# Performance work log

Hardware: AMD Instinct MI355X
Metric: run time of the kernel (lower is better)

The kernel has to match this reference:

```python
import jax, jax.numpy as jnp
import numpy as np

B, C, H, W, NW = 4, 32, 64, 64, 64
VMAX = 1.0


def _sunflower_mu_stddev(n, vmax, alpha=1.0):
    # sunflower seed arrangement on the complex plane (matches torch source)
    b = np.round(alpha * np.sqrt(n))
    phi = (np.sqrt(5.0) + 1.0) * 0.5
    k = np.arange(1, n + 1, dtype=np.float64)
    r = np.where(k > n - b, 1.0, np.sqrt(k - 0.5) / np.sqrt(n - (b + 1.0) / 2.0))
    theta = 2.0 * np.pi * k / phi ** 2
    mu = (r * np.cos(theta) + 1j * r * np.sin(theta)) * vmax
    # nearest-neighbor distance (replaces sklearn NearestNeighbors exactly)
    X = np.stack((mu.real, mu.imag), -1)  # (n,2)
    D = np.linalg.norm(X[:, None, :] - X[None, :, :], axis=-1)
    np.fill_diagonal(D, np.inf)
    nn_d = D.min(axis=1)
    stddev = (nn_d * nn_d).astype(np.float32)
    return mu.real.astype(np.float32), mu.imag.astype(np.float32), stddev


def setup_inputs() -> dict:
    key = jax.random.key(0)
    k1, k2, k3, k4 = jax.random.split(key, 4)
    mu_r, mu_i, stddev = _sunflower_mu_stddev(NW, VMAX)
    return {
        "x_real": jax.random.normal(k1, (B, C, H, W), dtype=jnp.float32),
        "x_imag": jax.random.normal(k2, (B, C, H, W), dtype=jnp.float32),
        "w_real": jax.random.normal(k3, (C, NW), dtype=jnp.float32) * 0.1,
        "w_imag": jax.random.normal(k4, (C, NW), dtype=jnp.float32) * 0.1,
        "b_real": jnp.zeros((1, C, 1), dtype=jnp.float32),
        "b_imag": jnp.zeros((1, C, 1), dtype=jnp.float32),
        "mu_real": jnp.asarray(mu_r),
        "mu_imag": jnp.asarray(mu_i),
        "stddev": jnp.asarray(stddev),
    }


def reference(x_real, x_imag, w_real, w_imag, b_real, b_imag, mu_real, mu_imag, stddev):
    Bb, Cc, Hh, Ww = x_real.shape
    # (B,C,HW,1) complex input vs (1,1,1,NW) complex centers
    xr = x_real.reshape(Bb, Cc, -1, 1)
    xi = x_imag.reshape(Bb, Cc, -1, 1)
    dr = xr - mu_real.reshape(1, 1, 1, -1)
    di = xi - mu_imag.reshape(1, 1, 1, -1)
    # conj(dist)*dist = |dist|^2 (real); exp of it is real-valued
    rbf = jnp.exp(-(dr * dr + di * di) / (2.0 * stddev))  # (B,C,HW,NW) real
    # complex channel-weighted reduction + complex bias
    out_r = jnp.einsum('abcd,bd->abc', rbf, w_real) + b_real
    out_i = jnp.einsum('abcd,bd->abc', rbf, w_imag) + b_imag
    # return real/imag stacked on last axis: (B,C,H,W,2)
    out = jnp.stack([out_r.reshape(Bb, Cc, Hh, Ww), out_i.reshape(Bb, Cc, Hh, Ww)], axis=-1)
    return out
```

## Files before the change

kernel.cpp:

```cpp
#include <hip/hip_runtime.h>

#define NB 4
#define NC 32
#define HW 4096
#define NW 64

#define PPT 4
#define TPB 256
#define PPB (PPT * TPB)
#define TILES (HW / PPB)

__global__ __launch_bounds__(TPB) void rbf_kernel(
    const float* __restrict__ x_real, const float* __restrict__ x_imag,
    const float* __restrict__ w_real, const float* __restrict__ w_imag,
    const float* __restrict__ b_real, const float* __restrict__ b_imag,
    const float* __restrict__ mu_real, const float* __restrict__ mu_imag,
    const float* __restrict__ stddev, float* __restrict__ out)
{
    const int bc   = blockIdx.x / TILES;
    const int tile = blockIdx.x % TILES;
    const int c    = bc % NC;
    const int t    = threadIdx.x;

    __shared__ float s_mu_r[NW], s_mu_i[NW], s_coef[NW], s_wr[NW], s_wi[NW];
    if (t < NW) {
        s_mu_r[t] = mu_real[t];
        s_mu_i[t] = mu_imag[t];
        s_coef[t] = -1.4426950408889634f / (2.0f * stddev[t]);
        s_wr[t]   = w_real[c * NW + t];
        s_wi[t]   = w_imag[c * NW + t];
    }
    __syncthreads();

    const int base = bc * HW + tile * PPB + t;

    float xr[PPT], xi[PPT], ar[PPT], ai[PPT];
#pragma unroll
    for (int p = 0; p < PPT; ++p) {
        xr[p] = x_real[base + p * TPB];
        xi[p] = x_imag[base + p * TPB];
        ar[p] = 0.0f;
        ai[p] = 0.0f;
    }

#pragma unroll 8
    for (int k = 0; k < NW; ++k) {
        const float mr = s_mu_r[k];
        const float mi = s_mu_i[k];
        const float cf = s_coef[k];
        const float wr = s_wr[k];
        const float wi = s_wi[k];
#pragma unroll
        for (int p = 0; p < PPT; ++p) {
            float dr  = xr[p] - mr;
            float di  = xi[p] - mi;
            float d2  = fmaf(di, di, dr * dr);
            float rbf = __builtin_amdgcn_exp2f(d2 * cf);
            ar[p] = fmaf(rbf, wr, ar[p]);
            ai[p] = fmaf(rbf, wi, ai[p]);
        }
    }

    const float br = b_real[c];
    const float bi = b_imag[c];
    float2* __restrict__ out2 = reinterpret_cast<float2*>(out);
#pragma unroll
    for (int p = 0; p < PPT; ++p) {
        out2[base + p * TPB] = make_float2(ar[p] + br, ai[p] + bi);
    }
}

extern "C" void kernel_launch(void* const* d_in, const int* in_sizes, int n_in,
                              void* d_out, int out_size, void* d_ws, size_t ws_size,
                              hipStream_t stream) {
    const float* x_real  = (const float*)d_in[0];
    const float* x_imag  = (const float*)d_in[1];
    const float* w_real  = (const float*)d_in[2];
    const float* w_imag  = (const float*)d_in[3];
    const float* b_real  = (const float*)d_in[4];
    const float* b_imag  = (const float*)d_in[5];
    const float* mu_real = (const float*)d_in[6];
    const float* mu_imag = (const float*)d_in[7];
    const float* stddev  = (const float*)d_in[8];
    float* out = (float*)d_out;

    const int grid = NB * NC * TILES;
    rbf_kernel<<<grid, TPB, 0, stream>>>(x_real, x_imag, w_real, w_imag,
                                         b_real, b_imag, mu_real, mu_imag,
                                         stddev, out);
}
```

Before: 79.23 us.

## Expand squared distance algebraically with precomputed per-center coefficient table

Rewrites the exponent cf*|x-mu|^2 as cf*|x|^2 - 2cf*mu·x + cf*|mu|^2, with per-center coefficients computed once by a small prep kernel into workspace. The inner loop then needs three FMAs per point instead of subtract/multiply/FMA/multiply. The change also drops shared memory and the block barrier in favour of broadcast global loads, halves points per thread, and vectorises the loads and stores. The expansion can lose precision through cancellation, and an extra kernel launch is added.

```diff
diff --git a/kernel.cpp b/kernel.cpp
--- a/kernel.cpp
+++ b/kernel.cpp
@@ -5,69 +5,75 @@
 #define HW 4096
 #define NW 64
 
-#define PPT 4
+#define PPT 2
 #define TPB 256
 #define PPB (PPT * TPB)
 #define TILES (HW / PPB)
+
+__global__ __launch_bounds__(64) void rbf_prep(
+    const float* __restrict__ mu_real, const float* __restrict__ mu_imag,
+    const float* __restrict__ stddev, float4* __restrict__ tab)
+{
+    const int k = threadIdx.x;
+    if (k < NW) {
+        const float mr = mu_real[k];
+        const float mi = mu_imag[k];
+        const float cf = -1.4426950408889634f / (2.0f * stddev[k]);
+        tab[k] = make_float4(cf, -2.0f * cf * mr, -2.0f * cf * mi,
+                             cf * fmaf(mr, mr, mi * mi));
+    }
+}
 
 __global__ __launch_bounds__(TPB) void rbf_kernel(
     const float* __restrict__ x_real, const float* __restrict__ x_imag,
     const float* __restrict__ w_real, const float* __restrict__ w_imag,
     const float* __restrict__ b_real, const float* __restrict__ b_imag,
-    const float* __restrict__ mu_real, const float* __restrict__ mu_imag,
-    const float* __restrict__ stddev, float* __restrict__ out)
+    const float4* __restrict__ tab, float* __restrict__ out)
 {
     const int bc   = blockIdx.x / TILES;
     const int tile = blockIdx.x % TILES;
     const int c    = bc % NC;
     const int t    = threadIdx.x;
 
-    __shared__ float s_mu_r[NW], s_mu_i[NW], s_coef[NW], s_wr[NW], s_wi[NW];
-    if (t < NW) {
-        s_mu_r[t] = mu_real[t];
-        s_mu_i[t] = mu_imag[t];
-        s_coef[t] = -1.4426950408889634f / (2.0f * stddev[t]);
-        s_wr[t]   = w_real[c * NW + t];
-        s_wi[t]   = w_imag[c * NW + t];
-    }
-    __syncthreads();
+    const int base = bc * HW + tile * PPB + 2 * t;
 
-    const int base = bc * HW + tile * PPB + t;
+    const float2 vr = *reinterpret_cast<const float2*>(x_real + base);
+    const float2 vi = *reinterpret_cast<const float2*>(x_imag + base);
+    const float xr0 = vr.x, xr1 = vr.y;
+    const float xi0 = vi.x, xi1 = vi.y;
+    const float r20 = fmaf(xr0, xr0, xi0 * xi0);
+    const float r21 = fmaf(xr1, xr1, xi1 * xi1);
 
-    float xr[PPT], xi[PPT], ar[PPT], ai[PPT];
-#pragma unroll
-    for (int p = 0; p < PPT; ++p) {
-        xr[p] = x_real[base + p * TPB];
-        xi[p] = x_imag[base + p * TPB];
-        ar[p] = 0.0f;
-        ai[p] = 0.0f;
-    }
+    const float br = b_real[c];
+    const float bi = b_imag[c];
+    float ar0 = br, ai0 = bi, ar1 = br, ai1 = bi;
+
+    const int cbase = c * NW;
 
 #pragma unroll 8
     for (int k = 0; k < NW; ++k) {
-        const float mr = s_mu_r[k];
-        const float mi = s_mu_i[k];
-        const float cf = s_coef[k];
-        const float wr = s_wr[k];
-        const float wi = s_wi[k];
-#pragma unroll
-        for (int p = 0; p < PPT; ++p) {
-            float dr  = xr[p] - mr;
-            float di  = xi[p] - mi;
-            float d2  = fmaf(di, di, dr * dr);
-            float rbf = __builtin_amdgcn_exp2f(d2 * cf);
-            ar[p] = fmaf(rbf, wr, ar[p]);
-            ai[p] = fmaf(rbf, wi, ai[p]);
-        }
+        const float4 cc = tab[k];
+        const float  wr = w_real[cbase + k];
+        const float  wi = w_imag[cbase + k];
+
+        float t0 = fmaf(cc.z, xi0, cc.w);
+        float t1 = fmaf(cc.z, xi1, cc.w);
+        t0 = fmaf(cc.y, xr0, t0);
+        t1 = fmaf(cc.y, xr1, t1);
+        t0 = fmaf(cc.x, r20, t0);
+        t1 = fmaf(cc.x, r21, t1);
+
+        const float e0 = __builtin_amdgcn_exp2f(t0);
+        const float e1 = __builtin_amdgcn_exp2f(t1);
+
+        ar0 = fmaf(e0, wr, ar0);
+        ai0 = fmaf(e0, wi, ai0);
+        ar1 = fmaf(e1, wr, ar1);
+        ai1 = fmaf(e1, wi, ai1);
     }
 
-    const float br = b_real[c];
-    const float bi = b_imag[c];
-    float2* __restrict__ out2 = reinterpret_cast<float2*>(out);
-#pragma unroll
-    for (int p = 0; p < PPT; ++p) {
-        out2[base + p * TPB] = make_float2(ar[p] + br, ai[p] + bi);
-    }
+    float4* __restrict__ o4 = reinterpret_cast<float4*>(out + 2 * base);
+    *o4 = make_float4(ar0, ai0, ar1, ai1);
 }
 
 extern "C" void kernel_launch(void* const* d_in, const int* in_sizes, int n_in,
@@ -82,10 +88,12 @@
     const float* mu_real = (const float*)d_in[6];
     const float* mu_imag = (const float*)d_in[7];
     const float* stddev  = (const float*)d_in[8];
-    float* out = (float*)d_out;
+    float* out  = (float*)d_out;
+    float4* tab = (float4*)d_ws;
+
+    rbf_prep<<<1, 64, 0, stream>>>(mu_real, mu_imag, stddev, tab);
 
     const int grid = NB * NC * TILES;
     rbf_kernel<<<grid, TPB, 0, stream>>>(x_real, x_imag, w_real, w_imag,
-                                         b_real, b_imag, mu_real, mu_imag,
-                                         stddev, out);
+                                         b_real, b_imag, tab, out);
 }
```

Result: no change. 77.98 us (-1.6%).
